# Kernel tuning notes

Measured on AMD Instinct MI355X. Metric: run time of the kernel, lower is better.

Reference implementation:

```python
import jax, jax.numpy as jnp
import numpy as np

N = 50000
K = 4
D_IN = 256
D_OUT = 64
E = 800000

def setup_inputs() -> dict:
    key = jax.random.key(0)
    k1, k2, k3, k4, k5 = jax.random.split(key, 5)
    x = jax.random.normal(k1, (N, K, D_IN), dtype=jnp.float32)
    weight = jax.random.normal(k2, (D_IN, D_OUT), dtype=jnp.float32) * (1.0 / np.sqrt(D_IN))
    adj_rows = jax.random.randint(k3, (E,), 0, N, dtype=jnp.int32)
    adj_cols = jax.random.randint(k4, (E,), 0, N, dtype=jnp.int32)
    adj_vals = jax.random.uniform(k5, (E,), dtype=jnp.float32)
    return {"x": x, "weight": weight, "adj_rows": adj_rows, "adj_cols": adj_cols, "adj_vals": adj_vals}

def reference(x, weight, adj_rows, adj_cols, adj_vals):
    # x: [N, K, D_in]; weight: [D_in, D_out]
    # dropout p=0.0 / eval mode -> identity
    # support = x @ W for every sample k, vectorized over K
    support = jnp.einsum('nkd,df->nkf', x, weight)          # [N, K, D_out]
    # sparse adj matmul: out[r] += vals[e] * support[cols[e]]
    msgs = adj_vals[:, None, None] * support[adj_cols]       # [E, K, D_out]
    out = jax.ops.segment_sum(msgs, adj_rows, num_segments=N)  # [N, K, D_out]
    return jax.nn.relu(out)
```

## Files before the change

kernel.cpp:

```cpp
#include <hip/hip_runtime.h>
#include <hip/hip_bf16.h>
#include <stdint.h>

#define D_IN   256
#define D_OUT  64
#define KHEADS 4
#define ROWLEN 256
#define GBM    128
#define LDWT   264
#define CAP    128

typedef __attribute__((ext_vector_type(8))) short bf16x8;
typedef __attribute__((ext_vector_type(4))) float f32x4;

__device__ __forceinline__ unsigned short f2bf(float f) {
  unsigned u = __float_as_uint(f);
  return (unsigned short)((u + 0x7fffu + ((u >> 16) & 1u)) >> 16);
}

__device__ __forceinline__ bf16x8 cvt_frag(float4 u, float4 v) {
  bf16x8 r;
  r[0] = (short)f2bf(u.x); r[1] = (short)f2bf(u.y);
  r[2] = (short)f2bf(u.z); r[3] = (short)f2bf(u.w);
  r[4] = (short)f2bf(v.x); r[5] = (short)f2bf(v.y);
  r[6] = (short)f2bf(v.z); r[7] = (short)f2bf(v.w);
  return r;
}

__global__ __launch_bounds__(256) void gemm_mfma(const float* __restrict__ X,
                                                 const float* __restrict__ W,
                                                 signed char* __restrict__ Sq,
                                                 float* __restrict__ scaleArr,
                                                 int M, int Nnodes) {
  __shared__ unsigned short lWt[64 * LDWT];
  const int t    = threadIdx.x;
  const int wave = t >> 6;
  const int lane = t & 63;
  const int q    = lane >> 4;
  const int l16  = lane & 15;
  const long row0 = (long)blockIdx.x * GBM;

  long r0 = row0 + wave * 32 + l16;
  long r1 = r0 + 16;
  if (r0 >= M) r0 = M - 1;
  if (r1 >= M) r1 = M - 1;
  const float* px0 = X + r0 * D_IN + q * 8;
  const float* px1 = X + r1 * D_IN + q * 8;

  float4 raw[8][2][2];
#pragma unroll
  for (int s = 0; s < 8; ++s) {
    raw[s][0][0] = *(const float4*)(px0 + s * 32);
    raw[s][0][1] = *(const float4*)(px0 + s * 32 + 4);
    raw[s][1][0] = *(const float4*)(px1 + s * 32);
    raw[s][1][1] = *(const float4*)(px1 + s * 32 + 4);
  }

#pragma unroll
  for (int j = 0; j < 16; ++j) {
    int flat = t + j * 256;
    int kr   = flat >> 4;
    int nn   = (flat & 15) << 2;
    float4 v = *(const float4*)&W[(size_t)kr * D_OUT + nn];
    lWt[(nn + 0) * LDWT + kr] = f2bf(v.x);
    lWt[(nn + 1) * LDWT + kr] = f2bf(v.y);
    lWt[(nn + 2) * LDWT + kr] = f2bf(v.z);
    lWt[(nn + 3) * LDWT + kr] = f2bf(v.w);
  }
  __syncthreads();

  f32x4 acc[2][4];
#pragma unroll
  for (int rb = 0; rb < 2; ++rb)
#pragma unroll
    for (int cb = 0; cb < 4; ++cb) acc[rb][cb] = (f32x4){0.f, 0.f, 0.f, 0.f};

#pragma unroll
  for (int s = 0; s < 8; ++s) {
    bf16x8 a0 = cvt_frag(raw[s][0][0], raw[s][0][1]);
    bf16x8 a1 = cvt_frag(raw[s][1][0], raw[s][1][1]);
#pragma unroll
    for (int cb = 0; cb < 4; ++cb) {
      bf16x8 b = *(const bf16x8*)&lWt[(cb * 16 + l16) * LDWT + s * 32 + q * 8];
      acc[0][cb] = __builtin_amdgcn_mfma_f32_16x16x32_bf16(a0, b, acc[0][cb], 0, 0, 0);
      acc[1][cb] = __builtin_amdgcn_mfma_f32_16x16x32_bf16(a1, b, acc[1][cb], 0, 0, 0);
    }
  }

  float nm0 = 0.f, nm1 = 0.f;
#pragma unroll
  for (int cb = 0; cb < 4; ++cb)
#pragma unroll
    for (int reg = 0; reg < 4; ++reg) {
      nm0 = fmaxf(nm0, fabsf(acc[0][cb][reg]));
      nm1 = fmaxf(nm1, fabsf(acc[1][cb][reg]));
    }
#pragma unroll
  for (int d = 1; d < 16; d <<= 1) {
    nm0 = fmaxf(nm0, __shfl_xor(nm0, d, 64));
    nm1 = fmaxf(nm1, __shfl_xor(nm1, d, 64));
  }
  const float inv0 = (nm0 > 0.f) ? 127.f / nm0 : 0.f;
  const float inv1 = (nm1 > 0.f) ? 127.f / nm1 : 0.f;
  const int node_base = blockIdx.x * 32 + wave * 8;
  if (l16 == 0) {
    int n0 = node_base + q;
    int n1 = node_base + 4 + q;
    if (n0 < Nnodes) scaleArr[n0] = nm0 / 127.f;
    if (n1 < Nnodes) scaleArr[n1] = nm1 / 127.f;
  }
#pragma unroll
  for (int rb = 0; rb < 2; ++rb) {
    const float inv = rb ? inv1 : inv0;
#pragma unroll
    for (int cb = 0; cb < 4; ++cb)
#pragma unroll
      for (int reg = 0; reg < 4; ++reg) {
        long r = row0 + wave * 32 + rb * 16 + q * 4 + reg;
        if (r < M) {
          int qi = (int)rintf(acc[rb][cb][reg] * inv);
          Sq[r * D_OUT + cb * 16 + l16] = (signed char)qi;
        }
      }
  }
}

__global__ __launch_bounds__(256) void place_kernel(const int* __restrict__ rows,
                                                    const int* __restrict__ cols,
                                                    const float* __restrict__ vals,
                                                    const float* __restrict__ scaleArr,
                                                    int* __restrict__ cnt,
                                                    uint2* __restrict__ ecv, int E) {
  int e = blockIdx.x * 256 + threadIdx.x;
  if (e < E) {
    int r = rows[e];
    int c = cols[e];
    float vp = vals[e] * scaleArr[c];
    int pos = atomicAdd(&cnt[r], 1);
    if (pos < CAP)
      ecv[((size_t)r << 7) + pos] = make_uint2((unsigned)c, __float_as_uint(vp));
  }
}

__global__ __launch_bounds__(256) void gather_kernel(const int* __restrict__ Sqi,
                                                     const int* __restrict__ cnt,
                                                     const uint2* __restrict__ ecv,
                                                     float* __restrict__ out, int n) {
  const int lane = threadIdx.x & 63;
  const int r = blockIdx.x * 4 + (threadIdx.x >> 6);
  if (r >= n) return;
  int deg = cnt[r];
  if (deg > CAP) deg = CAP;
  const uint2* __restrict__ bucket = ecv + ((size_t)r << 7);

  float4 acc[8];
#pragma unroll
  for (int j = 0; j < 8; ++j) acc[j] = make_float4(0.f, 0.f, 0.f, 0.f);

  for (int i = 0; i < deg; i += 8) {
    const int lim = deg - 1;
    unsigned col[8];
    float    val[8];
#pragma unroll
    for (int j = 0; j < 8; ++j) {
      int idx = i + j;
      uint2 e = bucket[idx <= lim ? idx : lim];
      col[j] = e.x;
      val[j] = (idx <= lim) ? __uint_as_float(e.y) : 0.f;
    }
    int wv[8];
#pragma unroll
    for (int j = 0; j < 8; ++j) wv[j] = Sqi[(size_t)col[j] * 64 + lane];
#pragma unroll
    for (int j = 0; j < 8; ++j) {
      acc[j].x += val[j] * (float)(wv[j] << 24 >> 24);
      acc[j].y += val[j] * (float)(wv[j] << 16 >> 24);
      acc[j].z += val[j] * (float)(wv[j] <<  8 >> 24);
      acc[j].w += val[j] * (float)(wv[j] >> 24);
    }
  }
  float4 res;
  res.x = fmaxf(acc[0].x + acc[1].x + acc[2].x + acc[3].x +
                acc[4].x + acc[5].x + acc[6].x + acc[7].x, 0.f);
  res.y = fmaxf(acc[0].y + acc[1].y + acc[2].y + acc[3].y +
                acc[4].y + acc[5].y + acc[6].y + acc[7].y, 0.f);
  res.z = fmaxf(acc[0].z + acc[1].z + acc[2].z + acc[3].z +
                acc[4].z + acc[5].z + acc[6].z + acc[7].z, 0.f);
  res.w = fmaxf(acc[0].w + acc[1].w + acc[2].w + acc[3].w +
                acc[4].w + acc[5].w + acc[6].w + acc[7].w, 0.f);
  *(float4*)&out[(size_t)r * ROWLEN + (lane << 2)] = res;
}

extern "C" void kernel_launch(void* const* d_in, const int* in_sizes, int n_in,
                              void* d_out, int out_size, void* d_ws, size_t ws_size,
                              hipStream_t stream) {
  const float* x    = (const float*)d_in[0];
  const float* w    = (const float*)d_in[1];
  const int*   rows = (const int*)d_in[2];
  const int*   cols = (const int*)d_in[3];
  const float* vals = (const float*)d_in[4];
  float* out = (float*)d_out;

  const int E = in_sizes[2];
  const int N = in_sizes[0] / (KHEADS * D_IN);
  const int M = N * KHEADS;

  char* ws = (char*)d_ws;
  size_t o = 0;
  signed char* Sq = (signed char*)(ws + o); o += (size_t)M * D_OUT;
  o = (o + 15) & ~(size_t)15;
  float* scaleArr = (float*)(ws + o); o += (size_t)N * sizeof(float);
  o = (o + 15) & ~(size_t)15;
  int* cnt = (int*)(ws + o); o += (size_t)N * sizeof(int);
  o = (o + 15) & ~(size_t)15;
  uint2* ecv = (uint2*)(ws + o);

  hipMemsetAsync(cnt, 0, (size_t)N * sizeof(int), stream);

  gemm_mfma<<<(M + GBM - 1) / GBM, 256, 0, stream>>>(x, w, Sq, scaleArr, M, N);
  place_kernel<<<(E + 255) / 256, 256, 0, stream>>>(rows, cols, vals, scaleArr, cnt, ecv, E);
  gather_kernel<<<(N + 3) / 4, 256, 0, stream>>>((const int*)Sq, cnt, ecv, out, N);
}
```

Baseline: 418.7 us.

## Stage X tiles through LDS in K-chunks instead of register-held rows

The GEMM kernel now loops over the 256-wide input dimension in chunks of 64. For each chunk it loads X and W cooperatively with coalesced float4 reads, converts them to bf16 into shared memory, and then reads MFMA fragments from LDS. Previously each lane preloaded its full rows of X into registers using strided per-lane reads. The change is meant to improve global load coalescing and cut register pressure, at the cost of extra LDS traffic and two barriers per chunk with no overlap between loading and compute.

```diff
diff --git a/kernel.cpp b/kernel.cpp
--- a/kernel.cpp
+++ b/kernel.cpp
@@ -7,7 +7,8 @@
 #define KHEADS 4
 #define ROWLEN 256
 #define GBM    128
-#define LDWT   264
+#define LDAB   72
+#define LDWB   72
 #define CAP    128
 
 typedef __attribute__((ext_vector_type(8))) short bf16x8;
@@ -16,15 +17,6 @@
 __device__ __forceinline__ unsigned short f2bf(float f) {
   unsigned u = __float_as_uint(f);
   return (unsigned short)((u + 0x7fffu + ((u >> 16) & 1u)) >> 16);
-}
-
-__device__ __forceinline__ bf16x8 cvt_frag(float4 u, float4 v) {
-  bf16x8 r;
-  r[0] = (short)f2bf(u.x); r[1] = (short)f2bf(u.y);
-  r[2] = (short)f2bf(u.z); r[3] = (short)f2bf(u.w);
-  r[4] = (short)f2bf(v.x); r[5] = (short)f2bf(v.y);
-  r[6] = (short)f2bf(v.z); r[7] = (short)f2bf(v.w);
-  return r;
 }
 
 __global__ __launch_bounds__(256) void gemm_mfma(const float* __restrict__ X,
@@ -32,7 +24,8 @@
                                                  signed char* __restrict__ Sq,
                                                  float* __restrict__ scaleArr,
                                                  int M, int Nnodes) {
-  __shared__ unsigned short lWt[64 * LDWT];
+  __shared__ unsigned short lA[GBM * LDAB];
+  __shared__ unsigned short lWt[64 * LDWB];
   const int t    = threadIdx.x;
   const int wave = t >> 6;
   const int lane = t & 63;
@@ -40,51 +33,50 @@
   const int l16  = lane & 15;
   const long row0 = (long)blockIdx.x * GBM;
 
-  long r0 = row0 + wave * 32 + l16;
-  long r1 = r0 + 16;
-  if (r0 >= M) r0 = M - 1;
-  if (r1 >= M) r1 = M - 1;
-  const float* px0 = X + r0 * D_IN + q * 8;
-  const float* px1 = X + r1 * D_IN + q * 8;
-
-  float4 raw[8][2][2];
-#pragma unroll
-  for (int s = 0; s < 8; ++s) {
-    raw[s][0][0] = *(const float4*)(px0 + s * 32);
-    raw[s][0][1] = *(const float4*)(px0 + s * 32 + 4);
-    raw[s][1][0] = *(const float4*)(px1 + s * 32);
-    raw[s][1][1] = *(const float4*)(px1 + s * 32 + 4);
-  }
-
-#pragma unroll
-  for (int j = 0; j < 16; ++j) {
-    int flat = t + j * 256;
-    int kr   = flat >> 4;
-    int nn   = (flat & 15) << 2;
-    float4 v = *(const float4*)&W[(size_t)kr * D_OUT + nn];
-    lWt[(nn + 0) * LDWT + kr] = f2bf(v.x);
-    lWt[(nn + 1) * LDWT + kr] = f2bf(v.y);
-    lWt[(nn + 2) * LDWT + kr] = f2bf(v.z);
-    lWt[(nn + 3) * LDWT + kr] = f2bf(v.w);
-  }
-  __syncthreads();
-
   f32x4 acc[2][4];
 #pragma unroll
   for (int rb = 0; rb < 2; ++rb)
 #pragma unroll
     for (int cb = 0; cb < 4; ++cb) acc[rb][cb] = (f32x4){0.f, 0.f, 0.f, 0.f};
 
-#pragma unroll
-  for (int s = 0; s < 8; ++s) {
-    bf16x8 a0 = cvt_frag(raw[s][0][0], raw[s][0][1]);
-    bf16x8 a1 = cvt_frag(raw[s][1][0], raw[s][1][1]);
-#pragma unroll
-    for (int cb = 0; cb < 4; ++cb) {
-      bf16x8 b = *(const bf16x8*)&lWt[(cb * 16 + l16) * LDWT + s * 32 + q * 8];
-      acc[0][cb] = __builtin_amdgcn_mfma_f32_16x16x32_bf16(a0, b, acc[0][cb], 0, 0, 0);
-      acc[1][cb] = __builtin_amdgcn_mfma_f32_16x16x32_bf16(a1, b, acc[1][cb], 0, 0, 0);
-    }
+  for (int k0 = 0; k0 < D_IN; k0 += 64) {
+#pragma unroll
+    for (int j = 0; j < 8; ++j) {
+      int flat = t + j * 256;
+      int r    = flat >> 4;
+      int kk   = (flat & 15) << 2;
+      long gr  = row0 + r;
+      if (gr >= M) gr = M - 1;
+      float4 v = *(const float4*)&X[gr * D_IN + k0 + kk];
+      ushort4 o;
+      o.x = f2bf(v.x); o.y = f2bf(v.y); o.z = f2bf(v.z); o.w = f2bf(v.w);
+      *(ushort4*)&lA[r * LDAB + kk] = o;
+    }
+#pragma unroll
+    for (int j = 0; j < 4; ++j) {
+      int flat = t + j * 256;
+      int kr   = flat >> 4;
+      int nn   = (flat & 15) << 2;
+      float4 v = *(const float4*)&W[(size_t)(k0 + kr) * D_OUT + nn];
+      lWt[(nn + 0) * LDWB + kr] = f2bf(v.x);
+      lWt[(nn + 1) * LDWB + kr] = f2bf(v.y);
+      lWt[(nn + 2) * LDWB + kr] = f2bf(v.z);
+      lWt[(nn + 3) * LDWB + kr] = f2bf(v.w);
+    }
+    __syncthreads();
+
+#pragma unroll
+    for (int s = 0; s < 2; ++s) {
+      bf16x8 a0 = *(const bf16x8*)&lA[(wave * 32 + 0  + l16) * LDAB + s * 32 + q * 8];
+      bf16x8 a1 = *(const bf16x8*)&lA[(wave * 32 + 16 + l16) * LDAB + s * 32 + q * 8];
+#pragma unroll
+      for (int cb = 0; cb < 4; ++cb) {
+        bf16x8 b = *(const bf16x8*)&lWt[(cb * 16 + l16) * LDWB + s * 32 + q * 8];
+        acc[0][cb] = __builtin_amdgcn_mfma_f32_16x16x32_bf16(a0, b, acc[0][cb], 0, 0, 0);
+        acc[1][cb] = __builtin_amdgcn_mfma_f32_16x16x32_bf16(a1, b, acc[1][cb], 0, 0, 0);
+      }
+    }
+    __syncthreads();
   }
 
   float nm0 = 0.f, nm1 = 0.f;
```

After: 407.9 us. 1.03x faster.
